# Optimization experiments

Measured on AMD Instinct MI355X. Metric: run time of the kernel, lower is better.

Reference implementation:

```python
import jax, jax.numpy as jnp
import numpy as np

T = 2048          # prefill tokens (bsz=1)
HID = 4096        # hidden_size
N_HEADS = 32
N_KV = 8
H_DIM = HID // N_HEADS  # 128
THETA = 10000.0


def _hadamard(n):
    H = np.array([[1.0]])
    while H.shape[0] < n:
        H = np.block([[H, H], [H, -H]])
    return (H / np.sqrt(n)).astype(np.float32)


def _quant_int4(x):
    # per-token symmetric int4 quantization (QuaRot Quantizer)
    s = jnp.max(jnp.abs(x), axis=-1, keepdims=True) / 7.0
    s = jnp.maximum(s, 1e-8)
    q = jnp.clip(jnp.round(x / s), -8.0, 7.0)
    return q, s


def _linear4bit(x, w_int, w_scale):
    # Linear4bit: quantize activation, int-int matmul, dequant with act & weight scales
    q, s = _quant_int4(x)
    return (q @ w_int.astype(jnp.float32).T) * s * w_scale[None, :]


def setup_inputs() -> dict:
    key = jax.random.key(0)
    ks = jax.random.split(key, 10)
    hidden_states = jax.random.normal(ks[0], (T, HID), jnp.float32)
    positions = jnp.arange(T, dtype=jnp.int32)

    def mkw(kw, kss, out_f):
        w = jax.random.randint(kw, (out_f, HID), -8, 8, jnp.int32).astype(jnp.int8)
        s = jax.random.uniform(kss, (out_f,), jnp.float32, minval=0.005, maxval=0.02)
        return w, s

    wq_int, wq_scale = mkw(ks[1], ks[2], N_HEADS * H_DIM)
    wk_int, wk_scale = mkw(ks[3], ks[4], N_KV * H_DIM)
    wv_int, wv_scale = mkw(ks[5], ks[6], N_KV * H_DIM)
    wo_int, wo_scale = mkw(ks[7], ks[8], HID)
    return dict(positions=positions, hidden_states=hidden_states,
                wq_int=wq_int, wq_scale=wq_scale,
                wk_int=wk_int, wk_scale=wk_scale,
                wv_int=wv_int, wv_scale=wv_scale,
                wo_int=wo_int, wo_scale=wo_scale)


def reference(positions, hidden_states, wq_int, wq_scale, wk_int, wk_scale,
              wv_int, wv_scale, wo_int, wo_scale):
    # int4 QKV projections
    q = _linear4bit(hidden_states, wq_int, wq_scale).reshape(T, N_HEADS, H_DIM)
    k = _linear4bit(hidden_states, wk_int, wk_scale).reshape(T, N_KV, H_DIM)
    v = _linear4bit(hidden_states, wv_int, wv_scale).reshape(T, N_KV, H_DIM)

    # neox-style RoPE
    half = H_DIM // 2
    inv_freq = 1.0 / (THETA ** (jnp.arange(0, H_DIM, 2, dtype=jnp.float32) / H_DIM))
    ang = positions.astype(jnp.float32)[:, None] * inv_freq  # [T, half]
    cos = jnp.cos(ang)[:, None, :]
    sin = jnp.sin(ang)[:, None, :]

    def rope(x):
        x1, x2 = x[..., :half], x[..., half:]
        return jnp.concatenate([x1 * cos - x2 * sin, x2 * cos + x1 * sin], axis=-1)

    q = rope(q)
    k = rope(k)

    # GQA: repeat KV heads
    rep = N_HEADS // N_KV
    k_r = jnp.repeat(k, rep, axis=1)  # [T, H, D]
    v_r = jnp.repeat(v, rep, axis=1)

    # causal attention
    scores = jnp.einsum('qhd,khd->hqk', q, k_r) * (H_DIM ** -0.5)
    causal = jnp.tril(jnp.ones((T, T), dtype=bool))
    scores = jnp.where(causal[None], scores, jnp.finfo(scores.dtype).min)
    probs = jax.nn.softmax(scores, axis=-1)
    attn = jnp.einsum('hqk,khd->qhd', probs, v_r)  # [T, H, D]

    # OnlineHadamard(num_heads): Hadamard transform across heads per (token, dim)
    H32 = jnp.asarray(_hadamard(N_HEADS))
    attn = jnp.einsum('qhd,gh->qgd', attn, H32).reshape(T, HID)

    # quantize then int4 o_proj
    qa, sa = _quant_int4(attn)
    out = (qa @ wo_int.astype(jnp.float32).T) * sa * wo_scale[None, :]
    return out
```

## Files before the change

kernel.cpp:

```cpp
#include <hip/hip_runtime.h>

#define T_SEQ 2048
#define HID 4096
#define NH 32
#define NKV 8
#define HD 128
#define KDIM 4096

typedef unsigned short u16;
typedef signed char s8;
typedef __attribute__((ext_vector_type(4))) float f32x4;
typedef __attribute__((ext_vector_type(4))) int i32x4;
typedef __attribute__((ext_vector_type(8))) short s16x8;
typedef __attribute__((ext_vector_type(4))) short s16x4;
typedef __attribute__((ext_vector_type(8))) __bf16 bf16x8;
typedef __attribute__((ext_vector_type(8))) _Float16 f16x8;

static __device__ __forceinline__ u16 f2bf(float f) {
    __bf16 b = (__bf16)f;
    return __builtin_bit_cast(unsigned short, b);
}
static __device__ __forceinline__ float bf2f(u16 b) {
    unsigned u = ((unsigned)b) << 16;
    return __builtin_bit_cast(float, u);
}
static __device__ __forceinline__ __bf16 bfbits(u16 b) {
    return __builtin_bit_cast(__bf16, b);
}
static __device__ __forceinline__ u16 f2h(float f) {
    _Float16 h = (_Float16)f;
    return __builtin_bit_cast(unsigned short, h);
}

typedef __attribute__((address_space(1))) const void gas_t;
typedef __attribute__((address_space(3))) void las_t;
static __device__ __forceinline__ void gll16(const void* g, void* l) {
    __builtin_amdgcn_global_load_lds((gas_t*)g, (las_t*)l, 16, 0, 0);
}

__global__ __launch_bounds__(256) void k_pre(const int* __restrict__ pos,
        const float* __restrict__ x, const int* __restrict__ wq,
        const int* __restrict__ wk, const int* __restrict__ wv,
        float* __restrict__ ctab, float* __restrict__ stab,
        s8* __restrict__ a8, float* __restrict__ srow,
        s8* __restrict__ q8, s8* __restrict__ k8, s8* __restrict__ v8) {
    int b = blockIdx.x, tid = threadIdx.x;
    if (b < 512) {
        int idx = b * 256 + tid;
        int t = idx >> 6, d = idx & 63;
        float p = (float)pos[t];
        float inv = (float)pow(10000.0, -(double)d / 64.0);
        float ang = p * inv;
        double dsn, dcs;
        sincos((double)ang, &dsn, &dcs);
        ctab[idx] = (float)dcs;
        stab[idx] = (float)dsn;
    } else if (b < 512 + 2048) {
        int row = b - 512;
        const float* xr = x + (size_t)row * HID;
        f32x4 v[4];
        float amax = 0.f;
#pragma unroll
        for (int i = 0; i < 4; ++i) {
            v[i] = *(const f32x4*)(xr + i * 1024 + tid * 4);
#pragma unroll
            for (int j = 0; j < 4; ++j) amax = fmaxf(amax, fabsf(v[i][j]));
        }
#pragma unroll
        for (int off = 32; off >= 1; off >>= 1)
            amax = fmaxf(amax, __shfl_xor(amax, off));
        __shared__ float red[4];
        if ((tid & 63) == 0) red[tid >> 6] = amax;
        __syncthreads();
        amax = fmaxf(fmaxf(red[0], red[1]), fmaxf(red[2], red[3]));
        float s = fmaxf(amax / 7.f, 1e-8f);
        if (tid == 0) srow[row] = s;
        int* qr = (int*)(a8 + (size_t)row * HID);
#pragma unroll
        for (int i = 0; i < 4; ++i) {
            int p = 0;
#pragma unroll
            for (int j = 0; j < 4; ++j) {
                float q = rintf(v[i][j] / s);
                q = fminf(fmaxf(q, -8.f), 7.f);
                p |= ((int)q & 0xff) << (8 * j);
            }
            qr[i * 256 + tid] = p;
        }
    } else {
        size_t i = ((size_t)(b - 2560) * 256 + tid) * 16;
        const int* src; s8* dst; size_t off;
        if (i < 16777216) { src = wq; dst = q8; off = i; }
        else if (i < 20971520) { src = wk; dst = k8; off = i - 16777216; }
        else { src = wv; dst = v8; off = i - 20971520; }
        i32x4 o;
#pragma unroll
        for (int j = 0; j < 4; ++j) {
            i32x4 v = *(const i32x4*)(src + off + j * 4);
            o[j] = (v[0] & 0xff) | ((v[1] & 0xff) << 8) |
                   ((v[2] & 0xff) << 16) | (v[3] << 24);
        }
        *(i32x4*)(dst + off) = o;
    }
}

__global__ __launch_bounds__(256) void k_w8(const int* __restrict__ w,
                                            s8* __restrict__ w8) {
    size_t i = ((size_t)blockIdx.x * 256 + threadIdx.x) * 16;
    i32x4 o;
#pragma unroll
    for (int j = 0; j < 4; ++j) {
        i32x4 v = *(const i32x4*)(w + i + j * 4);
        o[j] = (v[0] & 0xff) | ((v[1] & 0xff) << 8) | ((v[2] & 0xff) << 16) |
               (v[3] << 24);
    }
    *(i32x4*)(w8 + i) = o;
}

__global__ __launch_bounds__(256) void k_gemm8(const s8* __restrict__ A,
        const s8* __restrict__ W, const float* __restrict__ sRow,
        const float* __restrict__ sCol, float* __restrict__ outp,
        int M, int N, int K) {
    __shared__ __align__(16) s8 sA[16384], sB[16384];
    int tid = threadIdx.x;
    int brow = blockIdx.x * 128, bcol = blockIdx.y * 128;
    int wid = tid >> 6, lane = tid & 63;
    int wr = (wid >> 1) * 64, wc = (wid & 1) * 64;
    int lr = lane & 15, lc = lane >> 4;
    i32x4 acc[4][4] = {};
    for (int k0 = 0; k0 < K; k0 += 128) {
        __syncthreads();
#pragma unroll
        for (int j = 0; j < 4; ++j) {
            int base = wid * 1024 + j * 4096;
            int o = base + lane * 16;
            int r = o >> 7;
            int c = (o & 127) ^ ((r & 7) << 4);
            gll16(A + (size_t)(brow + r) * K + (k0 + c), (char*)sA + base);
            gll16(W + (size_t)(bcol + r) * K + (k0 + c), (char*)sB + base);
        }
        asm volatile("s_waitcnt vmcnt(0)" ::: "memory");
        __syncthreads();
#pragma unroll
        for (int kk = 0; kk < 2; ++kk) {
            i32x4 af[4], bf[4];
#pragma unroll
            for (int m = 0; m < 4; ++m) {
                int r = wr + m * 16 + lr;
                int sl = ((kk * 4 + lc) ^ (r & 7)) * 16;
                af[m] = *(const i32x4*)&sA[r * 128 + sl];
            }
#pragma unroll
            for (int n = 0; n < 4; ++n) {
                int r = wc + n * 16 + lr;
                int sl = ((kk * 4 + lc) ^ (r & 7)) * 16;
                bf[n] = *(const i32x4*)&sB[r * 128 + sl];
            }
#pragma unroll
            for (int m = 0; m < 4; ++m)
#pragma unroll
                for (int n = 0; n < 4; ++n)
                    acc[m][n] = __builtin_amdgcn_mfma_i32_16x16x64_i8(
                        af[m], bf[n], acc[m][n], 0, 0, 0);
        }
    }
#pragma unroll
    for (int m = 0; m < 4; ++m) {
        int row0 = brow + wr + m * 16 + lc * 4;
#pragma unroll
        for (int n = 0; n < 4; ++n) {
            int col = bcol + wc + n * 16 + lr;
            float scl = sCol[col];
#pragma unroll
            for (int r = 0; r < 4; ++r)
                outp[(size_t)(row0 + r) * N + col] =
                    (float)acc[m][n][r] * sRow[row0 + r] * scl;
        }
    }
}

__global__ __launch_bounds__(256) void k_gemmkv(const s8* __restrict__ A,
        const s8* __restrict__ Wk, const s8* __restrict__ Wv,
        const float* __restrict__ sRow, const float* __restrict__ sColK,
        const float* __restrict__ sColV, float* __restrict__ kout,
        u16* __restrict__ voutf) {
    __shared__ __align__(16) s8 sA[16384], sB[16384];
    int tid = threadIdx.x;
    int by = blockIdx.y;
    int isV = by >> 3;
    const s8* W = isV ? Wv : Wk;
    int brow = blockIdx.x * 128, bcol = (by & 7) * 128;
    const int K = KDIM, N = NKV * HD;
    int wid = tid >> 6, lane = tid & 63;
    int wr = (wid >> 1) * 64, wc = (wid & 1) * 64;
    int lr = lane & 15, lc = lane >> 4;
    i32x4 acc[4][4] = {};
    for (int k0 = 0; k0 < K; k0 += 128) {
        __syncthreads();
#pragma unroll
        for (int j = 0; j < 4; ++j) {
            int base = wid * 1024 + j * 4096;
            int o = base + lane * 16;
            int r = o >> 7;
            int c = (o & 127) ^ ((r & 7) << 4);
            gll16(A + (size_t)(brow + r) * K + (k0 + c), (char*)sA + base);
            gll16(W + (size_t)(bcol + r) * K + (k0 + c), (char*)sB + base);
        }
        asm volatile("s_waitcnt vmcnt(0)" ::: "memory");
        __syncthreads();
#pragma unroll
        for (int kk = 0; kk < 2; ++kk) {
            i32x4 af[4], bf[4];
#pragma unroll
            for (int m = 0; m < 4; ++m) {
                int r = wr + m * 16 + lr;
                int sl = ((kk * 4 + lc) ^ (r & 7)) * 16;
                af[m] = *(const i32x4*)&sA[r * 128 + sl];
            }
#pragma unroll
            for (int n = 0; n < 4; ++n) {
                int r = wc + n * 16 + lr;
                int sl = ((kk * 4 + lc) ^ (r & 7)) * 16;
                bf[n] = *(const i32x4*)&sB[r * 128 + sl];
            }
#pragma unroll
            for (int m = 0; m < 4; ++m)
#pragma unroll
                for (int n = 0; n < 4; ++n)
                    acc[m][n] = __builtin_amdgcn_mfma_i32_16x16x64_i8(
                        af[m], bf[n], acc[m][n], 0, 0, 0);
        }
    }
#pragma unroll
    for (int m = 0; m < 4; ++m) {
        int row0 = brow + wr + m * 16 + lc * 4;
#pragma unroll
        for (int n = 0; n < 4; ++n) {
            int col = bcol + wc + n * 16 + lr;
            if (!isV) {
                float scl = sColK[col];
#pragma unroll
                for (int r = 0; r < 4; ++r)
                    kout[(size_t)(row0 + r) * N + col] =
                        (float)acc[m][n][r] * sRow[row0 + r] * scl;
            } else {
                float scl = sColV[col];
                int kvh = col >> 7, d = col & 127;
                int nn = d >> 4, lrv = d & 15;
                int kt = row0 >> 6, rem = row0 & 63;
                int kc = rem >> 5, lcv = (rem & 31) >> 3, j0 = rem & 7;
                size_t base =
                    ((((size_t)(kvh * 32 + kt) * 2 + kc) * 8 + nn) * 64 +
                     lcv * 16 + lrv) * 8 + j0;
                s16x4 hh;
#pragma unroll
                for (int r = 0; r < 4; ++r) {
                    float val = (float)acc[m][n][r] * sRow[row0 + r] * scl;
                    hh[r] = (short)f2h(val);
                }
                *(s16x4*)(voutf + base) = hh;
            }
        }
    }
}

__global__ __launch_bounds__(256) void k_ropek(const float* __restrict__ kf,
        const float* __restrict__ ctab, const float* __restrict__ stab,
        u16* __restrict__ khf, u16* __restrict__ klf) {
    int t = blockIdx.x, tid = threadIdx.x;
    int kt = t >> 6, rem = t & 63, cblk = rem >> 4, lrk = rem & 15;
    for (int idx = tid; idx < NKV * 64; idx += 256) {
        int kh = idx >> 6, d = idx & 63;
        float cs = ctab[t * 64 + d], sn = stab[t * 64 + d];
        size_t base = (size_t)t * (NKV * HD) + kh * HD;
        float x1 = kf[base + d], x2 = kf[base + d + 64];
        float r1 = x1 * cs - x2 * sn;
        float r2 = x2 * cs + x1 * sn;
        size_t tb = (((size_t)(kh * 32 + kt) * 4 + cblk) * 4) * 512;
#pragma unroll
        for (int half = 0; half < 2; ++half) {
            int x = d + half * 64;
            float rv = half ? r2 : r1;
            int dcx = x >> 5, lcx = (x & 31) >> 3, jx = x & 7;
            size_t ii = tb + (size_t)dcx * 512 + (lcx * 16 + lrk) * 8 + jx;
            u16 hb = f2bf(rv);
            khf[ii] = hb;
            klf[ii] = f2bf(rv - bf2f(hb));
        }
    }
}

__global__ __launch_bounds__(512, 4) void k_attn(float* __restrict__ qf,
        const u16* __restrict__ khf, const u16* __restrict__ klf,
        const u16* __restrict__ vf,
        const float* __restrict__ ctab, const float* __restrict__ stab) {
    int bid = blockIdx.x;
    int lo = bid & 255, hi = bid >> 8;
    int h = lo & 31;
    int bx = hi ? 15 - (lo >> 5) : (lo >> 5);
    int kvh = h >> 2;
    int tid = threadIdx.x, wid = tid >> 6, lane = tid & 63;
    int lr = lane & 15, lc = lane >> 4;
    int q0 = bx * 128 + wid * 16, q_hi = q0 + 15;
    __shared__ __align__(16) u16 smem[37888];
    u16* pb = smem + 32768 + wid * 640;
    const float SCL = 0.12751744f;
    size_t kvbase = (size_t)kvh * 32 * 8192;
    auto stageK = [&](int kt) {
        const char* gk = (const char*)(khf + kvbase + (size_t)kt * 8192);
        const char* gl = (const char*)(klf + kvbase + (size_t)kt * 8192);
#pragma unroll
        for (int j = 0; j < 4; ++j) {
            int c = wid * 4 + j;
            int sel = c >> 4;
            int inner = (c & 15) * 1024;
            gll16((sel ? gl : gk) + inner + lane * 16,
                  (char*)smem + sel * 16384 + inner);
        }
    };
    auto stageV = [&](int kt, int buf) {
        const char* gv = (const char*)(vf + kvbase + (size_t)kt * 8192);
#pragma unroll
        for (int j = 0; j < 2; ++j) {
            int c = wid * 2 + j;
            gll16(gv + c * 1024 + lane * 16,
                  (char*)smem + 32768 + buf * 16384 + c * 1024);
        }
    };
    bf16x8 aqh[4], aql[4];
    {
        const float* qrow = qf + (size_t)(q0 + lr) * HID + h * HD;
        const float* ct = ctab + (size_t)(q0 + lr) * 64 + lc * 8;
        const float* st = stab + (size_t)(q0 + lr) * 64 + lc * 8;
        float qv[4][8];
#pragma unroll
        for (int dc = 0; dc < 4; ++dc) {
            f32x4 a = *(const f32x4*)(qrow + dc * 32 + lc * 8);
            f32x4 b = *(const f32x4*)(qrow + dc * 32 + lc * 8 + 4);
#pragma unroll
            for (int j = 0; j < 4; ++j) { qv[dc][j] = a[j]; qv[dc][j + 4] = b[j]; }
        }
        float cs[2][8], sn[2][8];
#pragma unroll
        for (int hf = 0; hf < 2; ++hf) {
            f32x4 c0 = *(const f32x4*)(ct + hf * 32);
            f32x4 c1 = *(const f32x4*)(ct + hf * 32 + 4);
            f32x4 s0 = *(const f32x4*)(st + hf * 32);
            f32x4 s1 = *(const f32x4*)(st + hf * 32 + 4);
#pragma unroll
            for (int j = 0; j < 4; ++j) {
                cs[hf][j] = c0[j]; cs[hf][j + 4] = c1[j];
                sn[hf][j] = s0[j]; sn[hf][j + 4] = s1[j];
            }
        }
#pragma unroll
        for (int dc0 = 0; dc0 < 2; ++dc0)
#pragma unroll
            for (int j = 0; j < 8; ++j) {
                float c = cs[dc0][j], s2 = sn[dc0][j];
                float x1 = qv[dc0][j], x2 = qv[dc0 + 2][j];
                qv[dc0][j] = x1 * c - x2 * s2;
                qv[dc0 + 2][j] = x2 * c + x1 * s2;
            }
#pragma unroll
        for (int dc = 0; dc < 4; ++dc)
#pragma unroll
            for (int j = 0; j < 8; ++j) {
                float v = qv[dc][j] * SCL;
                u16 hb = f2bf(v);
                aqh[dc][j] = bfbits(hb);
                aql[dc][j] = bfbits(f2bf(v - bf2f(hb)));
            }
    }
    f32x4 oacc[8] = {};
    float m = -1e30f, l = 0.f;
    int NT = 2 * bx + 2;
    stageK(0);
    stageV(0, 0);
    asm volatile("s_waitcnt vmcnt(0)" ::: "memory");
    __syncthreads();
    int cur = 0;
    for (int kt = 0; kt < NT; ++kt) {
        int k0 = kt * 64;
        f32x4 s[4] = {};
        __builtin_amdgcn_s_setprio(1);
#pragma unroll
        for (int c = 0; c < 4; ++c) {
            if (k0 + c * 16 <= q_hi) {
                f32x4 a = {};
#pragma unroll
                for (int dc = 0; dc < 4; ++dc) {
                    bf16x8 kh8 = *(const bf16x8*)&smem[((c * 4 + dc) * 64 + lane) * 8];
                    bf16x8 kl8 =
                        *(const bf16x8*)&smem[8192 + ((c * 4 + dc) * 64 + lane) * 8];
                    a = __builtin_amdgcn_mfma_f32_16x16x32_bf16(kh8, aqh[dc], a, 0, 0, 0);
                    a = __builtin_amdgcn_mfma_f32_16x16x32_bf16(kh8, aql[dc], a, 0, 0, 0);
                    a = __builtin_amdgcn_mfma_f32_16x16x32_bf16(kl8, aqh[dc], a, 0, 0, 0);
                }
                s[c] = a;
            }
        }
        __builtin_amdgcn_s_setprio(0);
        __syncthreads();
        if (kt + 1 < NT) {
            stageK(kt + 1);
            stageV(kt + 1, cur ^ 1);
        }
        int q = q0 + lr;
        float tmax = -1e30f;
#pragma unroll
        for (int c = 0; c < 4; ++c) {
            bool active = (k0 + c * 16 <= q_hi);
            bool edge = (k0 + c * 16 + 15 >= q0);
#pragma unroll
            for (int r = 0; r < 4; ++r) {
                float sv = active ? s[c][r] : -1e30f;
                if (active && edge) {
                    int key = k0 + c * 16 + lc * 4 + r;
                    if (key > q) sv = -1e30f;
                }
                s[c][r] = sv;
                tmax = fmaxf(tmax, sv);
            }
        }
        tmax = fmaxf(tmax, __shfl_xor(tmax, 16));
        tmax = fmaxf(tmax, __shfl_xor(tmax, 32));
        if (__any(tmax > m + 8.0f)) {
            float mn = fmaxf(m, tmax);
            float alpha = exp2f(m - mn);
            m = mn;
            l *= alpha;
            float a0 = __shfl(alpha, lc * 4 + 0);
            float a1 = __shfl(alpha, lc * 4 + 1);
            float a2 = __shfl(alpha, lc * 4 + 2);
            float a3 = __shfl(alpha, lc * 4 + 3);
#pragma unroll
            for (int n = 0; n < 8; ++n) {
                oacc[n][0] *= a0; oacc[n][1] *= a1;
                oacc[n][2] *= a2; oacc[n][3] *= a3;
            }
        }
        u16 pbf[4][4];
        float psum = 0.f;
#pragma unroll
        for (int c = 0; c < 4; ++c)
#pragma unroll
            for (int r = 0; r < 4; ++r) {
                float pv = exp2f(s[c][r] - m);
                _Float16 ph = (_Float16)pv;
                pbf[c][r] = __builtin_bit_cast(unsigned short, ph);
                psum += (float)ph;
            }
        psum += __shfl_xor(psum, 16);
        psum += __shfl_xor(psum, 32);
        l += psum;
#pragma unroll
        for (int kc = 0; kc < 2; ++kc) {
            if (k0 + kc * 32 <= q_hi) {
                s16x4 w0, w1;
#pragma unroll
                for (int r = 0; r < 4; ++r) {
                    w0[r] = (short)pbf[kc * 2][r];
                    w1[r] = (short)pbf[kc * 2 + 1][r];
                }
                *(s16x4*)&pb[lr * 40 + lc * 4] = w0;
                *(s16x4*)&pb[lr * 40 + 16 + lc * 4] = w1;
                asm volatile("s_waitcnt lgkmcnt(0)" ::: "memory");
                f16x8 pa = *(const f16x8*)&pb[lr * 40 + lc * 8];
                __builtin_amdgcn_s_setprio(1);
#pragma unroll
                for (int n = 0; n < 8; ++n) {
                    f16x8 v8 = *(const f16x8*)&smem[16384 + cur * 8192 +
                                                    ((kc * 8 + n) * 64 + lane) * 8];
                    oacc[n] = __builtin_amdgcn_mfma_f32_16x16x32_f16(pa, v8, oacc[n], 0, 0, 0);
                }
                __builtin_amdgcn_s_setprio(0);
            }
        }
        asm volatile("s_waitcnt vmcnt(0)" ::: "memory");
        __syncthreads();
        cur ^= 1;
    }
    float l0 = __shfl(l, lc * 4 + 0);
    float l1 = __shfl(l, lc * 4 + 1);
    float l2 = __shfl(l, lc * 4 + 2);
    float l3 = __shfl(l, lc * 4 + 3);
#pragma unroll
    for (int n = 0; n < 8; ++n) {
        int col = h * HD + n * 16 + lr;
        qf[(size_t)(q0 + lc * 4 + 0) * HID + col] = oacc[n][0] / l0;
        qf[(size_t)(q0 + lc * 4 + 1) * HID + col] = oacc[n][1] / l1;
        qf[(size_t)(q0 + lc * 4 + 2) * HID + col] = oacc[n][2] / l2;
        qf[(size_t)(q0 + lc * 4 + 3) * HID + col] = oacc[n][3] / l3;
    }
}

__global__ __launch_bounds__(256) void k_hadq(const float* __restrict__ attn,
        s8* __restrict__ a2, float* __restrict__ sa) {
    int t = blockIdx.x, tid = threadIdx.x;
    int w = tid >> 6, lane = tid & 63;
    int d = (w & 1) * 64 + lane;
    int half = w >> 1;
    __shared__ float rowb[HID];
    const float* ar = attn + (size_t)t * HID;
#pragma unroll
    for (int i = 0; i < 4; ++i)
        *(f32x4*)&rowb[i * 1024 + tid * 4] = *(const f32x4*)(ar + i * 1024 + tid * 4);
    __syncthreads();
    float u[16];
#pragma unroll
    for (int i = 0; i < 16; ++i) u[i] = rowb[(half * 16 + i) * 128 + d];
#pragma unroll
    for (int s = 1; s < 16; s <<= 1)
#pragma unroll
        for (int i = 0; i < 16; ++i)
            if (!(i & s)) {
                float a = u[i], b = u[i | s];
                u[i] = a + b;
                u[i | s] = a - b;
            }
#pragma unroll
    for (int i = 0; i < 16; ++i) rowb[(half * 16 + i) * 128 + d] = u[i];
    __syncthreads();
    float y[16], amax = 0.f;
#pragma unroll
    for (int i = 0; i < 16; ++i) {
        float o = rowb[((half ^ 1) * 16 + i) * 128 + d];
        float yv = half ? (o - u[i]) : (u[i] + o);
        yv *= 0.17677669529663687f;
        y[i] = yv;
        amax = fmaxf(amax, fabsf(yv));
    }
#pragma unroll
    for (int off = 32; off >= 1; off >>= 1)
        amax = fmaxf(amax, __shfl_xor(amax, off));
    __shared__ float red[4];
    if ((tid & 63) == 0) red[tid >> 6] = amax;
    __syncthreads();
    amax = fmaxf(fmaxf(red[0], red[1]), fmaxf(red[2], red[3]));
    float s = fmaxf(amax / 7.f, 1e-8f);
    if (tid == 0) sa[t] = s;
    s8* o2 = a2 + (size_t)t * HID;
#pragma unroll
    for (int i = 0; i < 16; ++i) {
        float q = rintf(y[i] / s);
        q = fminf(fmaxf(q, -8.f), 7.f);
        o2[(half * 16 + i) * 128 + d] = (s8)(int)q;
    }
}

extern "C" void kernel_launch(void* const* d_in, const int* in_sizes, int n_in,
                              void* d_out, int out_size, void* d_ws, size_t ws_size,
                              hipStream_t stream) {
    const int* positions = (const int*)d_in[0];
    const float* hidden = (const float*)d_in[1];
    const int* wq = (const int*)d_in[2];
    const float* wq_s = (const float*)d_in[3];
    const int* wk = (const int*)d_in[4];
    const float* wk_s = (const float*)d_in[5];
    const int* wv = (const int*)d_in[6];
    const float* wv_s = (const float*)d_in[7];
    const int* wo = (const int*)d_in[8];
    const float* wo_s = (const float*)d_in[9];

    char* ws = (char*)d_ws;
    float* s_x = (float*)(ws);
    float* s_a = (float*)(ws + 8192);
    float* ctab = (float*)(ws + 16384);
    float* stab = (float*)(ws + 16384 + 524288);
    char* base1 = ws + 16384 + 1048576;
    s8* a8 = (s8*)base1;
    float* q_f = (float*)(base1 + 8388608);
    float* k_f = (float*)(base1 + 8388608 + 33554432);
    char* X = base1 + 8388608 + 33554432 + 8388608;
    char* W2 = X + 16777216;
    s8* wq8 = (s8*)X;
    u16* khf = (u16*)(X);
    u16* klf = (u16*)(X + 4194304);
    u16* vf = (u16*)(X + 8388608);
    s8* wk8 = (s8*)W2;
    s8* wv8 = (s8*)(W2 + 4194304);
    s8* wo8 = (s8*)X;

    k_pre<<<8704, 256, 0, stream>>>(positions, hidden, wq, wk, wv, ctab, stab,
                                    a8, s_x, wq8, wk8, wv8);
    k_gemm8<<<dim3(16, 32), 256, 0, stream>>>(a8, wq8, s_x, wq_s, q_f,
                                              T_SEQ, HID, KDIM);
    k_gemmkv<<<dim3(16, 16), 256, 0, stream>>>(a8, wk8, wv8, s_x, wk_s, wv_s,
                                               k_f, vf);
    k_ropek<<<T_SEQ, 256, 0, stream>>>(k_f, ctab, stab, khf, klf);
    k_attn<<<512, 512, 0, stream>>>(q_f, khf, klf, vf, ctab, stab);
    k_w8<<<4096, 256, 0, stream>>>(wo, wo8);
    k_hadq<<<T_SEQ, 256, 0, stream>>>(q_f, a8, s_a);
    k_gemm8<<<dim3(16, 32), 256, 0, stream>>>(a8, wo8, s_a, wo_s,
                                              (float*)d_out, T_SEQ, HID, KDIM);
}
```

Baseline: 299.1 us.

## Double-buffer int8 GEMMs, merge QKV launches, fold Wo packing into Hadamard kernel

```diff
diff --git a/kernel.cpp b/kernel.cpp
--- a/kernel.cpp
+++ b/kernel.cpp
@@ -104,43 +104,42 @@
     }
 }
 
-__global__ __launch_bounds__(256) void k_w8(const int* __restrict__ w,
-                                            s8* __restrict__ w8) {
-    size_t i = ((size_t)blockIdx.x * 256 + threadIdx.x) * 16;
-    i32x4 o;
-#pragma unroll
-    for (int j = 0; j < 4; ++j) {
-        i32x4 v = *(const i32x4*)(w + i + j * 4);
-        o[j] = (v[0] & 0xff) | ((v[1] & 0xff) << 8) | ((v[2] & 0xff) << 16) |
-               (v[3] << 24);
-    }
-    *(i32x4*)(w8 + i) = o;
-}
-
-__global__ __launch_bounds__(256) void k_gemm8(const s8* __restrict__ A,
-        const s8* __restrict__ W, const float* __restrict__ sRow,
-        const float* __restrict__ sCol, float* __restrict__ outp,
-        int M, int N, int K) {
-    __shared__ __align__(16) s8 sA[16384], sB[16384];
+__global__ __launch_bounds__(256) void k_qkv(const s8* __restrict__ A,
+        const s8* __restrict__ Wq, const s8* __restrict__ Wk,
+        const s8* __restrict__ Wv, const float* __restrict__ sRow,
+        const float* __restrict__ sq, const float* __restrict__ sk,
+        const float* __restrict__ sv, float* __restrict__ qout,
+        float* __restrict__ kout, u16* __restrict__ voutf) {
+    __shared__ __align__(16) s8 sA[2][16384], sB[2][16384];
     int tid = threadIdx.x;
-    int brow = blockIdx.x * 128, bcol = blockIdx.y * 128;
+    int by = blockIdx.y;
+    int mode = by < 32 ? 0 : (by < 40 ? 1 : 2);
+    const s8* W = mode == 0 ? Wq : (mode == 1 ? Wk : Wv);
+    const float* sCol = mode == 0 ? sq : (mode == 1 ? sk : sv);
+    int bcolb = mode == 0 ? by : (mode == 1 ? by - 32 : by - 40);
+    int brow = blockIdx.x * 128, bcol = bcolb * 128;
+    const int K = KDIM;
     int wid = tid >> 6, lane = tid & 63;
     int wr = (wid >> 1) * 64, wc = (wid & 1) * 64;
     int lr = lane & 15, lc = lane >> 4;
     i32x4 acc[4][4] = {};
-    for (int k0 = 0; k0 < K; k0 += 128) {
-        __syncthreads();
+    auto stage = [&](int buf, int k0) {
 #pragma unroll
         for (int j = 0; j < 4; ++j) {
             int base = wid * 1024 + j * 4096;
             int o = base + lane * 16;
             int r = o >> 7;
             int c = (o & 127) ^ ((r & 7) << 4);
-            gll16(A + (size_t)(brow + r) * K + (k0 + c), (char*)sA + base);
-            gll16(W + (size_t)(bcol + r) * K + (k0 + c), (char*)sB + base);
-        }
-        asm volatile("s_waitcnt vmcnt(0)" ::: "memory");
-        __syncthreads();
+            gll16(A + (size_t)(brow + r) * K + (k0 + c), (char*)sA[buf] + base);
+            gll16(W + (size_t)(bcol + r) * K + (k0 + c), (char*)sB[buf] + base);
+        }
+    };
+    stage(0, 0);
+    asm volatile("s_waitcnt vmcnt(0)" ::: "memory");
+    __syncthreads();
+    int cur = 0;
+    for (int k0 = 0; k0 < K; k0 += 128) {
+        if (k0 + 128 < K) stage(cur ^ 1, k0 + 128);
 #pragma unroll
         for (int kk = 0; kk < 2; ++kk) {
             i32x4 af[4], bf[4];
@@ -148,13 +147,13 @@
             for (int m = 0; m < 4; ++m) {
                 int r = wr + m * 16 + lr;
                 int sl = ((kk * 4 + lc) ^ (r & 7)) * 16;
-                af[m] = *(const i32x4*)&sA[r * 128 + sl];
+                af[m] = *(const i32x4*)&sA[cur][r * 128 + sl];
             }
 #pragma unroll
             for (int n = 0; n < 4; ++n) {
                 int r = wc + n * 16 + lr;
                 int sl = ((kk * 4 + lc) ^ (r & 7)) * 16;
-                bf[n] = *(const i32x4*)&sB[r * 128 + sl];
+                bf[n] = *(const i32x4*)&sB[cur][r * 128 + sl];
             }
 #pragma unroll
             for (int m = 0; m < 4; ++m)
@@ -163,6 +162,9 @@
                     acc[m][n] = __builtin_amdgcn_mfma_i32_16x16x64_i8(
                         af[m], bf[n], acc[m][n], 0, 0, 0);
         }
+        asm volatile("s_waitcnt vmcnt(0)" ::: "memory");
+        __syncthreads();
+        cur ^= 1;
     }
 #pragma unroll
     for (int m = 0; m < 4; ++m) {
@@ -171,80 +173,17 @@
         for (int n = 0; n < 4; ++n) {
             int col = bcol + wc + n * 16 + lr;
             float scl = sCol[col];
-#pragma unroll
-            for (int r = 0; r < 4; ++r)
-                outp[(size_t)(row0 + r) * N + col] =
-                    (float)acc[m][n][r] * sRow[row0 + r] * scl;
-        }
-    }
-}
-
-__global__ __launch_bounds__(256) void k_gemmkv(const s8* __restrict__ A,
-        const s8* __restrict__ Wk, const s8* __restrict__ Wv,
-        const float* __restrict__ sRow, const float* __restrict__ sColK,
-        const float* __restrict__ sColV, float* __restrict__ kout,
-        u16* __restrict__ voutf) {
-    __shared__ __align__(16) s8 sA[16384], sB[16384];
-    int tid = threadIdx.x;
-    int by = blockIdx.y;
-    int isV = by >> 3;
-    const s8* W = isV ? Wv : Wk;
-    int brow = blockIdx.x * 128, bcol = (by & 7) * 128;
-    const int K = KDIM, N = NKV * HD;
-    int wid = tid >> 6, lane = tid & 63;
-    int wr = (wid >> 1) * 64, wc = (wid & 1) * 64;
-    int lr = lane & 15, lc = lane >> 4;
-    i32x4 acc[4][4] = {};
-    for (int k0 = 0; k0 < K; k0 += 128) {
-        __syncthreads();
-#pragma unroll
-        for (int j = 0; j < 4; ++j) {
-            int base = wid * 1024 + j * 4096;
-            int o = base + lane * 16;
-            int r = o >> 7;
-            int c = (o & 127) ^ ((r & 7) << 4);
-            gll16(A + (size_t)(brow + r) * K + (k0 + c), (char*)sA + base);
-            gll16(W + (size_t)(bcol + r) * K + (k0 + c), (char*)sB + base);
-        }
-        asm volatile("s_waitcnt vmcnt(0)" ::: "memory");
-        __syncthreads();
-#pragma unroll
-        for (int kk = 0; kk < 2; ++kk) {
-            i32x4 af[4], bf[4];
-#pragma unroll
-            for (int m = 0; m < 4; ++m) {
-                int r = wr + m * 16 + lr;
-                int sl = ((kk * 4 + lc) ^ (r & 7)) * 16;
-                af[m] = *(const i32x4*)&sA[r * 128 + sl];
-            }
-#pragma unroll
-            for (int n = 0; n < 4; ++n) {
-                int r = wc + n * 16 + lr;
-                int sl = ((kk * 4 + lc) ^ (r & 7)) * 16;
-                bf[n] = *(const i32x4*)&sB[r * 128 + sl];
-            }
-#pragma unroll
-            for (int m = 0; m < 4; ++m)
-#pragma unroll
-                for (int n = 0; n < 4; ++n)
-                    acc[m][n] = __builtin_amdgcn_mfma_i32_16x16x64_i8(
-                        af[m], bf[n], acc[m][n], 0, 0, 0);
-        }
-    }
-#pragma unroll
-    for (int m = 0; m < 4; ++m) {
-        int row0 = brow + wr + m * 16 + lc * 4;
-#pragma unroll
-        for (int n = 0; n < 4; ++n) {
-            int col = bcol + wc + n * 16 + lr;
-            if (!isV) {
-                float scl = sColK[col];
+            if (mode == 0) {
 #pragma unroll
                 for (int r = 0; r < 4; ++r)
-                    kout[(size_t)(row0 + r) * N + col] =
+                    qout[(size_t)(row0 + r) * HID + col] =
+                        (float)acc[m][n][r] * sRow[row0 + r] * scl;
+            } else if (mode == 1) {
+#pragma unroll
+                for (int r = 0; r < 4; ++r)
+                    kout[(size_t)(row0 + r) * (NKV * HD) + col] =
                         (float)acc[m][n][r] * sRow[row0 + r] * scl;
             } else {
-                float scl = sColV[col];
                 int kvh = col >> 7, d = col & 127;
                 int nn = d >> 4, lrv = d & 15;
                 int kt = row0 >> 6, rem = row0 & 63;
@@ -260,6 +199,75 @@
                 }
                 *(s16x4*)(voutf + base) = hh;
             }
+        }
+    }
+}
+
+__global__ __launch_bounds__(256) void k_gemm8(const s8* __restrict__ A,
+        const s8* __restrict__ W, const float* __restrict__ sRow,
+        const float* __restrict__ sCol, float* __restrict__ outp) {
+    __shared__ __align__(16) s8 sA[2][16384], sB[2][16384];
+    int tid = threadIdx.x;
+    int brow = blockIdx.x * 128, bcol = blockIdx.y * 128;
+    const int K = KDIM;
+    int wid = tid >> 6, lane = tid & 63;
+    int wr = (wid >> 1) * 64, wc = (wid & 1) * 64;
+    int lr = lane & 15, lc = lane >> 4;
+    i32x4 acc[4][4] = {};
+    auto stage = [&](int buf, int k0) {
+#pragma unroll
+        for (int j = 0; j < 4; ++j) {
+            int base = wid * 1024 + j * 4096;
+            int o = base + lane * 16;
+            int r = o >> 7;
+            int c = (o & 127) ^ ((r & 7) << 4);
+            gll16(A + (size_t)(brow + r) * K + (k0 + c), (char*)sA[buf] + base);
+            gll16(W + (size_t)(bcol + r) * K + (k0 + c), (char*)sB[buf] + base);
+        }
+    };
+    stage(0, 0);
+    asm volatile("s_waitcnt vmcnt(0)" ::: "memory");
+    __syncthreads();
+    int cur = 0;
+    for (int k0 = 0; k0 < K; k0 += 128) {
+        if (k0 + 128 < K) stage(cur ^ 1, k0 + 128);
+#pragma unroll
+        for (int kk = 0; kk < 2; ++kk) {
+            i32x4 af[4], bf[4];
+#pragma unroll
+            for (int m = 0; m < 4; ++m) {
+                int r = wr + m * 16 + lr;
+                int sl = ((kk * 4 + lc) ^ (r & 7)) * 16;
+                af[m] = *(const i32x4*)&sA[cur][r * 128 + sl];
+            }
+#pragma unroll
+            for (int n = 0; n < 4; ++n) {
+                int r = wc + n * 16 + lr;
+                int sl = ((kk * 4 + lc) ^ (r & 7)) * 16;
+                bf[n] = *(const i32x4*)&sB[cur][r * 128 + sl];
+            }
+#pragma unroll
+            for (int m = 0; m < 4; ++m)
+#pragma unroll
+                for (int n = 0; n < 4; ++n)
+                    acc[m][n] = __builtin_amdgcn_mfma_i32_16x16x64_i8(
+                        af[m], bf[n], acc[m][n], 0, 0, 0);
+        }
+        asm volatile("s_waitcnt vmcnt(0)" ::: "memory");
+        __syncthreads();
+        cur ^= 1;
+    }
+#pragma unroll
+    for (int m = 0; m < 4; ++m) {
+        int row0 = brow + wr + m * 16 + lc * 4;
+#pragma unroll
+        for (int n = 0; n < 4; ++n) {
+            int col = bcol + wc + n * 16 + lr;
+            float scl = sCol[col];
+#pragma unroll
+            for (int r = 0; r < 4; ++r)
+                outp[(size_t)(row0 + r) * HID + col] =
+                    (float)acc[m][n][r] * sRow[row0 + r] * scl;
         }
     }
 }
@@ -382,6 +390,7 @@
     int cur = 0;
     for (int kt = 0; kt < NT; ++kt) {
         int k0 = kt * 64;
+        if (kt + 1 < NT) stageV(kt + 1, cur ^ 1);
         f32x4 s[4] = {};
         __builtin_amdgcn_s_setprio(1);
 #pragma unroll
@@ -402,10 +411,7 @@
         }
         __builtin_amdgcn_s_setprio(0);
         __syncthreads();
-        if (kt + 1 < NT) {
-            stageK(kt + 1);
-            stageV(kt + 1, cur ^ 1);
-        }
+        if (kt + 1 < NT) stageK(kt + 1);
         int q = q0 + lr;
         float tmax = -1e30f;
 #pragma unroll
@@ -496,8 +502,24 @@
 }
 
 __global__ __launch_bounds__(256) void k_hadq(const float* __restrict__ attn,
-        s8* __restrict__ a2, float* __restrict__ sa) {
+        s8* __restrict__ a2, float* __restrict__ sa,
+        const int* __restrict__ wo, s8* __restrict__ wo8) {
     int t = blockIdx.x, tid = threadIdx.x;
+    {
+        size_t u0 = ((size_t)t * 256 + tid) * 2;
+#pragma unroll
+        for (int k = 0; k < 2; ++k) {
+            size_t i = (u0 + k) * 16;
+            i32x4 o;
+#pragma unroll
+            for (int j = 0; j < 4; ++j) {
+                i32x4 v = *(const i32x4*)(wo + i + j * 4);
+                o[j] = (v[0] & 0xff) | ((v[1] & 0xff) << 8) |
+                       ((v[2] & 0xff) << 16) | (v[3] << 24);
+            }
+            *(i32x4*)(wo8 + i) = o;
+        }
+    }
     int w = tid >> 6, lane = tid & 63;
     int d = (w & 1) * 64 + lane;
     int half = w >> 1;
@@ -584,14 +606,11 @@
 
     k_pre<<<8704, 256, 0, stream>>>(positions, hidden, wq, wk, wv, ctab, stab,
                                     a8, s_x, wq8, wk8, wv8);
-    k_gemm8<<<dim3(16, 32), 256, 0, stream>>>(a8, wq8, s_x, wq_s, q_f,
-                                              T_SEQ, HID, KDIM);
-    k_gemmkv<<<dim3(16, 16), 256, 0, stream>>>(a8, wk8, wv8, s_x, wk_s, wv_s,
-                                               k_f, vf);
+    k_qkv<<<dim3(16, 48), 256, 0, stream>>>(a8, wq8, wk8, wv8, s_x,
+                                            wq_s, wk_s, wv_s, q_f, k_f, vf);
     k_ropek<<<T_SEQ, 256, 0, stream>>>(k_f, ctab, stab, khf, klf);
     k_attn<<<512, 512, 0, stream>>>(q_f, khf, klf, vf, ctab, stab);
-    k_w8<<<4096, 256, 0, stream>>>(wo, wo8);
-    k_hadq<<<T_SEQ, 256, 0, stream>>>(q_f, a8, s_a);
+    k_hadq<<<T_SEQ, 256, 0, stream>>>(q_f, a8, s_a, wo, wo8);
     k_gemm8<<<dim3(16, 32), 256, 0, stream>>>(a8, wo8, s_a, wo_s,
-                                              (float*)d_out, T_SEQ, HID, KDIM);
-}
+                                              (float*)d_out);
+}
```

Measured after the change: 276.9 us. 7.4% less time.
